# Optimization experiments

Hardware: AMD Instinct MI355X
Metric: run time of the kernel (lower is better)

Reference implementation:

```python
import jax, jax.numpy as jnp
import numpy as np

THRESHOLD = 0.5
N_SEG = 5
NEG_INF = -1e30
EPS = 1e-12  # F.normalize eps


def setup_inputs() -> dict:
    key = jax.random.key(0)
    kx, kl = jax.random.split(key)
    B, D, L = 4096, 512, 80
    x = jax.random.normal(kx, (B, D), dtype=jnp.float32)
    labels = jax.random.randint(kl, (B, L), 0, 2, dtype=jnp.int32)
    return {"x": x, "labels": labels}


def reference(x, labels):
    B = x.shape[0]
    labels_f = labels.astype(jnp.float32)
    # pairwise Jaccard over multi-hot labels
    intersection = labels_f @ labels_f.T                      # [B, B]
    counts = labels_f.sum(axis=1, keepdims=True)              # [B, 1]
    union = counts + counts.T - intersection
    jaccard = intersection / union                            # [B, B]
    # cosine similarity (F.normalize with eps clamp)
    norm = jnp.maximum(jnp.linalg.norm(x, axis=1, keepdims=True), EPS)
    nx = x / norm
    sim = nx @ nx.T                                           # [B, B]
    # --- sample positive (uniform among jaccard > threshold), fixed key ---
    pos_mask = jaccard > THRESHOLD
    valid_mask = jnp.any(pos_mask, axis=1)                    # [B]
    logits = jnp.where(pos_mask, 0.0, NEG_INF)
    sampled = jax.random.categorical(jax.random.key(42), logits, axis=-1)
    pos_samples = jnp.where(valid_mask, sampled, 0)           # invalid rows -> 0
    # --- top-k negatives: jaccard strictly below the positive's jaccard ---
    pos_sim_j = jaccard[jnp.arange(B), pos_samples]           # [B]
    neg_mask = jaccard < pos_sim_j[:, None]
    neg_sims = jnp.where(neg_mask, jaccard, -jnp.inf)
    _, neg_samples = jax.lax.top_k(neg_sims, N_SEG)           # [B, N_SEG]
    # --- contrastive loss on cosine sims at sampled indices ---
    rel_pos = sim[jnp.arange(B), pos_samples]                 # [B]
    rel_neg = jnp.take_along_axis(sim, neg_samples, axis=1)   # [B, N_SEG]
    exp_pos = jnp.exp(rel_pos)
    sum_exp_neg = jnp.exp(rel_neg).sum(axis=1)
    loss = -jnp.log(exp_pos / (exp_pos + sum_exp_neg))
    vm = valid_mask.astype(x.dtype)
    return (loss * vm).sum() / vm.sum()
```

## Files before the change

kernel.cpp:

```cpp
#include <hip/hip_runtime.h>
#include <stdint.h>

#define B_ROWS 4096
#define DIMS   512
#define NLAB   80
#define HALF_ROWS 2048
#define HCNT   8388608u
#define CHUNK  1024
#define SEGCAP 256u

typedef unsigned long long u64;

__device__ __forceinline__ uint32_t rotl32(uint32_t x, uint32_t d) {
    return (x << d) | (x >> (32u - d));
}

__device__ __forceinline__ void tf2x32_key42(uint32_t c0, uint32_t c1,
                                             uint32_t& o0, uint32_t& o1) {
    const uint32_t ks0 = 0u;
    const uint32_t ks1 = 42u;
    const uint32_t ks2 = 0x1BD11BDAu ^ 0u ^ 42u;
    uint32_t x0 = c0 + ks0;
    uint32_t x1 = c1 + ks1;
#define TF_RND(r) { x0 += x1; x1 = rotl32(x1, (r)); x1 ^= x0; }
    TF_RND(13u) TF_RND(15u) TF_RND(26u) TF_RND(6u)
    x0 += ks1; x1 += ks2 + 1u;
    TF_RND(17u) TF_RND(29u) TF_RND(16u) TF_RND(24u)
    x0 += ks2; x1 += ks0 + 2u;
    TF_RND(13u) TF_RND(15u) TF_RND(26u) TF_RND(6u)
    x0 += ks0; x1 += ks1 + 3u;
    TF_RND(17u) TF_RND(29u) TF_RND(16u) TF_RND(24u)
    x0 += ks1; x1 += ks2 + 4u;
    TF_RND(13u) TF_RND(15u) TF_RND(26u) TF_RND(6u)
    x0 += ks2; x1 += ks0 + 5u;
#undef TF_RND
    o0 = x0; o1 = x1;
}

__device__ __forceinline__ u64 shflx64(u64 v, int m) {
    uint32_t lo = __shfl_xor((uint32_t)(v & 0xFFFFFFFFull), m, 64);
    uint32_t hi = __shfl_xor((uint32_t)(v >> 32), m, 64);
    return ((u64)hi << 32) | (u64)lo;
}

__device__ __forceinline__ uint32_t umx(uint32_t a, uint32_t b) { return a > b ? a : b; }
__device__ __forceinline__ uint32_t umn(uint32_t a, uint32_t b) { return a < b ? a : b; }

__device__ __forceinline__ void ins5_u32(uint32_t* t, uint32_t k) {
    t[4] = umx(t[4], k);
    uint32_t hi, lo;
    hi = umx(t[3], t[4]); lo = umn(t[3], t[4]); t[3] = hi; t[4] = lo;
    hi = umx(t[2], t[3]); lo = umn(t[2], t[3]); t[2] = hi; t[3] = lo;
    hi = umx(t[1], t[2]); lo = umn(t[1], t[2]); t[1] = hi; t[2] = lo;
    hi = umx(t[0], t[1]); lo = umn(t[0], t[1]); t[0] = hi; t[1] = lo;
}

__device__ __forceinline__ void merge5_u32(uint32_t* A, const uint32_t* Bv) {
    uint32_t a0=A[0],a1=A[1],a2=A[2],a3=A[3],a4=A[4];
    uint32_t b0=Bv[0],b1=Bv[1],b2=Bv[2],b3=Bv[3],b4=Bv[4];
    uint32_t m0 = umx(a0, b0);
    uint32_t m1 = umx(umx(a1, b1), umn(a0, b0));
    uint32_t m2 = umx(umx(a2, b2), umx(umn(a0, b1), umn(a1, b0)));
    uint32_t m3 = umx(umx(a3, b3), umx(umx(umn(a0, b2), umn(a1, b1)), umn(a2, b0)));
    uint32_t m4 = umx(umx(a4, b4), umx(umx(umn(a0, b3), umn(a1, b2)),
                                       umx(umn(a2, b1), umn(a3, b0))));
    A[0]=m0; A[1]=m1; A[2]=m2; A[3]=m3; A[4]=m4;
}

__device__ __forceinline__ uint32_t jkey19(uint32_t it, uint32_t u) {
    const uint32_t n = it << 19;
    float f = (float)it * __builtin_amdgcn_rcpf((float)u) * 524288.0f;
    uint32_t ak = (uint32_t)f;
    int r = (int)(n - ak * u);
    if (r < 0) { ak--; r += (int)u; }
    if (r >= (int)u) ak++;
    return ak + 1u;
}


__global__ __launch_bounds__(256) void prep_kernel(const float* __restrict__ x,
                                                   const int* __restrict__ labels,
                                                   uint4* __restrict__ pk,
                                                   float* __restrict__ norms) {
    const int tid = threadIdx.x;
    const int lane = tid & 63;
    const int row = blockIdx.x * 4 + (tid >> 6);
    const int* lr = labels + (size_t)row * NLAB;
    const int la = lr[lane];
    const int lb = (lane < 16) ? lr[64 + lane] : 0;
    const u64 b0 = __ballot(la != 0);
    const u64 b1 = __ballot(lb != 0);
    const uint32_t w2 = (uint32_t)b1 & 0xFFFFu;
    const uint32_t cnt = (uint32_t)__popcll(b0) + (uint32_t)__popc(w2);
    if (lane == 0) pk[row] = make_uint4((uint32_t)b0, (uint32_t)(b0 >> 32), w2, cnt);
    const float* xr = x + (size_t)row * DIMS;
    float ss = 0.f;
#pragma unroll
    for (int u = 0; u < 8; ++u) { float v = xr[lane + 64 * u]; ss += v * v; }
#pragma unroll
    for (int m = 1; m < 64; m <<= 1) ss += __shfl_xor(ss, m, 64);
    if (lane == 0) norms[row] = fmaxf(sqrtf(ss), 1e-12f);
}

__global__ __launch_bounds__(256) void fused_kernel(const float* __restrict__ x,
                                                    const uint4* __restrict__ pk,
                                                    const float* __restrict__ norms,
                                                    float2* __restrict__ blockPart) {
    __shared__ uint32_t segL[2][4][SEGCAP];
    __shared__ uint32_t cntL[2][4];
    __shared__ uint32_t keysL[2][4][5];
    __shared__ uint32_t tgL[2][6];
    __shared__ uint32_t validL[2];
    __shared__ float    simsL[2][6];
    __shared__ float    lossW[2], cntW2[2];

    const int tid = threadIdx.x;
    const int lane = tid & 63;
    const int sub  = tid >> 6;
    const int pr   = (int)blockIdx.x;
    const int r0 = pr, r1 = pr + HALF_ROWS;
    const uint4 P0 = pk[r0], P1 = pk[r1];
    const uint32_t cw0 = P0.w, cw1 = P1.w;
    const int jbase = sub * CHUNK;

    uint32_t cnt0 = 0u, cnt1 = 0u;
    uint32_t t0[5], t1[5];
#pragma unroll
    for (int k = 0; k < 5; ++k) {
        const uint32_t fk = (uint32_t)(~(jbase + k)) & 0xFFFu;
        t0[k] = fk; t1[k] = fk;
    }
    uint32_t thr0 = umx(t0[4] >> 12, 1u) - 1u;
    uint32_t thr1 = umx(t1[4] >> 12, 1u) - 1u;

#pragma unroll 4
    for (int jb = 0; jb < CHUNK; jb += 64) {
        const int j = jbase + jb + lane;
        const uint4 pj = pk[j];
        const uint32_t cj = pj.w;
        const uint32_t jx = (~(uint32_t)j) & 0xFFFu;
        const uint32_t it0 = (uint32_t)(__popc(P0.x & pj.x) + __popc(P0.y & pj.y) + __popc(P0.z & pj.z));
        const uint32_t u0  = cw0 + cj - it0;
        const uint32_t it1 = (uint32_t)(__popc(P1.x & pj.x) + __popc(P1.y & pj.y) + __popc(P1.z & pj.z));
        const uint32_t u1  = cw1 + cj - it1;
        const bool c0 = (it0 << 1) > u0;
        const bool c1 = (it1 << 1) > u1;
        const u64 bal0 = __ballot(c0);
        const u64 bal1 = __ballot(c1);
        const u64 lmask = (1ull << lane) - 1ull;
        if (c0) {
            const uint32_t off = cnt0 + (uint32_t)__popcll(bal0 & lmask);
            if (off < SEGCAP) segL[0][sub][off] = (it0 << 20) | (u0 << 12) | (uint32_t)j;
        } else if ((it0 << 19) >= __umul24(thr0, u0)) {
            ins5_u32(t0, (jkey19(it0, u0) << 12) | jx);
            thr0 = umx(t0[4] >> 12, 1u) - 1u;
        }
        cnt0 += (uint32_t)__popcll(bal0);
        if (c1) {
            const uint32_t off = cnt1 + (uint32_t)__popcll(bal1 & lmask);
            if (off < SEGCAP) segL[1][sub][off] = (it1 << 20) | (u1 << 12) | (uint32_t)j;
        } else if ((it1 << 19) >= __umul24(thr1, u1)) {
            ins5_u32(t1, (jkey19(it1, u1) << 12) | jx);
            thr1 = umx(t1[4] >> 12, 1u) - 1u;
        }
        cnt1 += (uint32_t)__popcll(bal1);
    }
#pragma unroll
    for (int m = 1; m < 64; m <<= 1) {
        uint32_t o[5];
#pragma unroll
        for (int k = 0; k < 5; ++k) o[k] = __shfl_xor(t0[k], m, 64);
        merge5_u32(t0, o);
#pragma unroll
        for (int k = 0; k < 5; ++k) o[k] = __shfl_xor(t1[k], m, 64);
        merge5_u32(t1, o);
    }
    if (lane == 0) {
        cntL[0][sub] = cnt0; cntL[1][sub] = cnt1;
#pragma unroll
        for (int k = 0; k < 5; ++k) { keysL[0][sub][k] = t0[k]; keysL[1][sub][k] = t1[k]; }
    }
    __syncthreads();

    if (sub < 2) {
        const int h = sub;
        uint32_t f[5];
#pragma unroll
        for (int k = 0; k < 5; ++k) f[k] = keysL[h][0][k];
#pragma unroll
        for (int s = 1; s < 4; ++s) {
            uint32_t o[5];
#pragma unroll
            for (int k = 0; k < 5; ++k) o[k] = keysL[h][s][k];
            merge5_u32(f, o);
        }
        uint32_t ns[4];
#pragma unroll
        for (int s = 0; s < 4; ++s) ns[s] = umn(cntL[h][s], SEGCAP);

        const uint32_t base23 = (uint32_t)pr * (uint32_t)B_ROWS;
        u64 gb = 0ull;
#pragma unroll
        for (int s = 0; s < 4; ++s) {
            for (int e = lane; e < (int)ns[s]; e += 64) {
                const uint32_t ent = segL[h][s][e];
                const uint32_t j  = ent & 0xFFFu;
                const uint32_t u  = (ent >> 12) & 0xFFu;
                const uint32_t it = ent >> 20;
                uint32_t o0, o1;
                tf2x32_key42(base23 + j, base23 + j + HCNT, o0, o1);
                const uint32_t o = h ? o1 : o0;
                const u64 key = ((u64)(o >> 9) << 41) | ((u64)((~j) & 0xFFFu) << 29) | (u64)jkey19(it, u);
                if (key > gb) gb = key;
            }
        }
#pragma unroll
        for (int m = 1; m < 64; m <<= 1) {
            const u64 o = shflx64(gb, m);
            if (o > gb) gb = o;
        }
        const bool valid = gb != 0ull;
        const int pos = valid ? (int)((~(uint32_t)(gb >> 29)) & 0xFFFu) : 0;
        const uint32_t pjkey = (uint32_t)(gb & 0xFFFFFu);

        uint32_t ts[5] = {0u, 0u, 0u, 0u, 0u};
#pragma unroll
        for (int s = 0; s < 4; ++s) {
            for (int e = lane; e < (int)ns[s]; e += 64) {
                const uint32_t ent = segL[h][s][e];
                const uint32_t j  = ent & 0xFFFu;
                const uint32_t u  = (ent >> 12) & 0xFFu;
                const uint32_t it = ent >> 20;
                const uint32_t k19 = jkey19(it, u);
                if (k19 < pjkey) ins5_u32(ts, (k19 << 12) | ((~j) & 0xFFFu));
            }
        }
#pragma unroll
        for (int m = 1; m < 64; m <<= 1) {
            uint32_t o[5];
#pragma unroll
            for (int k = 0; k < 5; ++k) o[k] = __shfl_xor(ts[k], m, 64);
            merge5_u32(ts, o);
        }
        merge5_u32(f, ts);

        if (lane == 0) {
            tgL[h][0] = (uint32_t)pos;
#pragma unroll
            for (int k = 0; k < 5; ++k) tgL[h][k + 1] = (~f[k]) & 0xFFFu;
            validL[h] = valid ? 1u : 0u;
        }
    }
    __syncthreads();

#pragma unroll
    for (int k = 0; k < 3; ++k) {
        const int d = sub + 4 * k;
        const int h = (d >= 6) ? 1 : 0;
        const int q = d - 6 * h;
        const int row = h ? r1 : r0;
        const int tgt = (int)tgL[h][q];
        const float* pa = x + (size_t)row * DIMS;
        const float* pb = x + (size_t)tgt * DIMS;
        float s = 0.f;
#pragma unroll
        for (int u = 0; u < 8; ++u) s += pa[lane + 64 * u] * pb[lane + 64 * u];
#pragma unroll
        for (int m = 1; m < 64; m <<= 1) s += __shfl_xor(s, m, 64);
        if (lane == 0) simsL[h][q] = s;
    }
    __syncthreads();

    if (sub < 2 && lane == 0) {
        const int h = sub;
        float loss = 0.f, cnt = 0.f;
        if (validL[h]) {
            const int row = h ? r1 : r0;
            const float nr = norms[row];
            const float sp = simsL[h][0] / (nr * norms[tgL[h][0]]);
            float sen = 0.f;
#pragma unroll
            for (int q = 1; q < 6; ++q) sen += expf(simsL[h][q] / (nr * norms[tgL[h][q]]));
            const float ep = expf(sp);
            loss = -logf(ep / (ep + sen));
            cnt = 1.f;
        }
        lossW[h] = loss; cntW2[h] = cnt;
    }
    __syncthreads();
    if (tid == 0) blockPart[pr] = make_float2(lossW[0] + lossW[1], cntW2[0] + cntW2[1]);
}

__global__ __launch_bounds__(256) void final_kernel(const float2* __restrict__ blockPart,
                                                    float* __restrict__ out) {
    __shared__ float rl[4], rc[4];
    const int tid = threadIdx.x;
    const int lane = tid & 63;
    const int w = tid >> 6;
    float sl = 0.f, sc = 0.f;
#pragma unroll
    for (int k = 0; k < 8; ++k) {
        const float2 p = blockPart[tid + 256 * k];
        sl += p.x; sc += p.y;
    }
#pragma unroll
    for (int m = 1; m < 64; m <<= 1) {
        sl += __shfl_xor(sl, m, 64);
        sc += __shfl_xor(sc, m, 64);
    }
    if (lane == 0) { rl[w] = sl; rc[w] = sc; }
    __syncthreads();
    if (tid == 0) out[0] = (rl[0] + rl[1] + rl[2] + rl[3]) / (rc[0] + rc[1] + rc[2] + rc[3]);
}

extern "C" void kernel_launch(void* const* d_in, const int* in_sizes, int n_in,
                              void* d_out, int out_size, void* d_ws, size_t ws_size,
                              hipStream_t stream) {
    const float* x      = (const float*)d_in[0];
    const int*   labels = (const int*)d_in[1];
    float* out = (float*)d_out;

    char* ws = (char*)d_ws;
    uint4*  pk    = (uint4*)ws;
    float*  norms = (float*)(ws + 65536);
    float2* bPart = (float2*)(ws + 65536 + 16384);

    hipLaunchKernelGGL(prep_kernel,  dim3(1024), dim3(256), 0, stream, x, labels, pk, norms);
    hipLaunchKernelGGL(fused_kernel, dim3(2048), dim3(256), 0, stream, x, pk, norms, bPart);
    hipLaunchKernelGGL(final_kernel, dim3(1),    dim3(256), 0, stream, bPart, out);
}
```

Baseline: 100.9 us.

## Process one row per block and spread the positive search across all warps

The fused kernel now handles one row per block instead of two, launching twice as many blocks. The positive-sampling and negative top-k scans over the segment list are now spread across all four warps, where before only two warps did them serially over all segments. The row vector is cached in registers for the six dot products. This shortens the serial tail inside each block and raises parallelism, at the cost of reloading the pk scan data per row and an extra block barrier.

```diff
diff --git a/kernel.cpp b/kernel.cpp
--- a/kernel.cpp
+++ b/kernel.cpp
@@ -105,193 +105,176 @@
 __global__ __launch_bounds__(256) void fused_kernel(const float* __restrict__ x,
                                                     const uint4* __restrict__ pk,
                                                     const float* __restrict__ norms,
-                                                    float2* __restrict__ blockPart) {
-    __shared__ uint32_t segL[2][4][SEGCAP];
-    __shared__ uint32_t cntL[2][4];
-    __shared__ uint32_t keysL[2][4][5];
-    __shared__ uint32_t tgL[2][6];
-    __shared__ uint32_t validL[2];
-    __shared__ float    simsL[2][6];
-    __shared__ float    lossW[2], cntW2[2];
+                                                    float2* __restrict__ rowPart) {
+    __shared__ uint32_t segL[4][SEGCAP];
+    __shared__ uint32_t cntL[4];
+    __shared__ uint32_t keysL[4][5];
+    __shared__ u64      gbL[4];
+    __shared__ uint32_t tsL[4][5];
+    __shared__ float    simsL[6];
 
     const int tid = threadIdx.x;
     const int lane = tid & 63;
     const int sub  = tid >> 6;
-    const int pr   = (int)blockIdx.x;
-    const int r0 = pr, r1 = pr + HALF_ROWS;
-    const uint4 P0 = pk[r0], P1 = pk[r1];
-    const uint32_t cw0 = P0.w, cw1 = P1.w;
+    const int row  = (int)blockIdx.x;
+    const int pr   = row & (HALF_ROWS - 1);
+    const int half = row >> 11;
+    const uint4 P = pk[row];
+    const uint32_t cw = P.w;
     const int jbase = sub * CHUNK;
 
-    uint32_t cnt0 = 0u, cnt1 = 0u;
-    uint32_t t0[5], t1[5];
-#pragma unroll
-    for (int k = 0; k < 5; ++k) {
-        const uint32_t fk = (uint32_t)(~(jbase + k)) & 0xFFFu;
-        t0[k] = fk; t1[k] = fk;
-    }
-    uint32_t thr0 = umx(t0[4] >> 12, 1u) - 1u;
-    uint32_t thr1 = umx(t1[4] >> 12, 1u) - 1u;
+    uint32_t cnt = 0u;
+    uint32_t t[5];
+#pragma unroll
+    for (int k = 0; k < 5; ++k) t[k] = (uint32_t)(~(jbase + k)) & 0xFFFu;
+    uint32_t thr = umx(t[4] >> 12, 1u) - 1u;
 
 #pragma unroll 4
     for (int jb = 0; jb < CHUNK; jb += 64) {
         const int j = jbase + jb + lane;
         const uint4 pj = pk[j];
-        const uint32_t cj = pj.w;
-        const uint32_t jx = (~(uint32_t)j) & 0xFFFu;
-        const uint32_t it0 = (uint32_t)(__popc(P0.x & pj.x) + __popc(P0.y & pj.y) + __popc(P0.z & pj.z));
-        const uint32_t u0  = cw0 + cj - it0;
-        const uint32_t it1 = (uint32_t)(__popc(P1.x & pj.x) + __popc(P1.y & pj.y) + __popc(P1.z & pj.z));
-        const uint32_t u1  = cw1 + cj - it1;
-        const bool c0 = (it0 << 1) > u0;
-        const bool c1 = (it1 << 1) > u1;
-        const u64 bal0 = __ballot(c0);
-        const u64 bal1 = __ballot(c1);
-        const u64 lmask = (1ull << lane) - 1ull;
-        if (c0) {
-            const uint32_t off = cnt0 + (uint32_t)__popcll(bal0 & lmask);
-            if (off < SEGCAP) segL[0][sub][off] = (it0 << 20) | (u0 << 12) | (uint32_t)j;
-        } else if ((it0 << 19) >= __umul24(thr0, u0)) {
-            ins5_u32(t0, (jkey19(it0, u0) << 12) | jx);
-            thr0 = umx(t0[4] >> 12, 1u) - 1u;
+        const uint32_t it = (uint32_t)(__popc(P.x & pj.x) + __popc(P.y & pj.y) + __popc(P.z & pj.z));
+        const uint32_t u  = cw + pj.w - it;
+        const bool c = (it << 1) > u;
+        const u64 bal = __ballot(c);
+        if (c) {
+            const uint32_t off = cnt + (uint32_t)__popcll(bal & ((1ull << lane) - 1ull));
+            if (off < SEGCAP) segL[sub][off] = (it << 20) | (u << 12) | (uint32_t)j;
+        } else if ((it << 19) >= __umul24(thr, u)) {
+            ins5_u32(t, (jkey19(it, u) << 12) | ((~(uint32_t)j) & 0xFFFu));
+            thr = umx(t[4] >> 12, 1u) - 1u;
         }
-        cnt0 += (uint32_t)__popcll(bal0);
-        if (c1) {
-            const uint32_t off = cnt1 + (uint32_t)__popcll(bal1 & lmask);
-            if (off < SEGCAP) segL[1][sub][off] = (it1 << 20) | (u1 << 12) | (uint32_t)j;
-        } else if ((it1 << 19) >= __umul24(thr1, u1)) {
-            ins5_u32(t1, (jkey19(it1, u1) << 12) | jx);
-            thr1 = umx(t1[4] >> 12, 1u) - 1u;
-        }
-        cnt1 += (uint32_t)__popcll(bal1);
+        cnt += (uint32_t)__popcll(bal);
     }
 #pragma unroll
     for (int m = 1; m < 64; m <<= 1) {
         uint32_t o[5];
 #pragma unroll
-        for (int k = 0; k < 5; ++k) o[k] = __shfl_xor(t0[k], m, 64);
-        merge5_u32(t0, o);
-#pragma unroll
-        for (int k = 0; k < 5; ++k) o[k] = __shfl_xor(t1[k], m, 64);
-        merge5_u32(t1, o);
+        for (int k = 0; k < 5; ++k) o[k] = __shfl_xor(t[k], m, 64);
+        merge5_u32(t, o);
     }
     if (lane == 0) {
-        cntL[0][sub] = cnt0; cntL[1][sub] = cnt1;
-#pragma unroll
-        for (int k = 0; k < 5; ++k) { keysL[0][sub][k] = t0[k]; keysL[1][sub][k] = t1[k]; }
-    }
-    __syncthreads();
-
+        cntL[sub] = cnt;
+#pragma unroll
+        for (int k = 0; k < 5; ++k) keysL[sub][k] = t[k];
+    }
+    __syncthreads();
+
+    const uint32_t nseg = umn(cntL[sub], SEGCAP);
+    const uint32_t base23 = (uint32_t)pr * (uint32_t)B_ROWS;
+    u64 gb = 0ull;
+    for (int e = lane; e < (int)nseg; e += 64) {
+        const uint32_t ent = segL[sub][e];
+        const uint32_t j  = ent & 0xFFFu;
+        const uint32_t u  = (ent >> 12) & 0xFFu;
+        const uint32_t it = ent >> 20;
+        uint32_t o0, o1;
+        tf2x32_key42(base23 + j, base23 + j + HCNT, o0, o1);
+        const uint32_t o = half ? o1 : o0;
+        const u64 key = ((u64)(o >> 9) << 41) | ((u64)((~j) & 0xFFFu) << 29) | (u64)jkey19(it, u);
+        if (key > gb) gb = key;
+    }
+#pragma unroll
+    for (int m = 1; m < 64; m <<= 1) {
+        const u64 o = shflx64(gb, m);
+        if (o > gb) gb = o;
+    }
+    if (lane == 0) gbL[sub] = gb;
+    __syncthreads();
+    u64 GB = gbL[0];
+#pragma unroll
+    for (int s = 1; s < 4; ++s) { const u64 o = gbL[s]; if (o > GB) GB = o; }
+    const bool valid = GB != 0ull;
+    const int pos = valid ? (int)((~(uint32_t)(GB >> 29)) & 0xFFFu) : 0;
+    const uint32_t pjkey = (uint32_t)(GB & 0xFFFFFu);
+
+    uint32_t ts[5] = {0u, 0u, 0u, 0u, 0u};
+    for (int e = lane; e < (int)nseg; e += 64) {
+        const uint32_t ent = segL[sub][e];
+        const uint32_t j  = ent & 0xFFFu;
+        const uint32_t u  = (ent >> 12) & 0xFFu;
+        const uint32_t it = ent >> 20;
+        const uint32_t k19 = jkey19(it, u);
+        if (k19 < pjkey) ins5_u32(ts, (k19 << 12) | ((~j) & 0xFFFu));
+    }
+#pragma unroll
+    for (int m = 1; m < 64; m <<= 1) {
+        uint32_t o[5];
+#pragma unroll
+        for (int k = 0; k < 5; ++k) o[k] = __shfl_xor(ts[k], m, 64);
+        merge5_u32(ts, o);
+    }
+    if (lane == 0) {
+#pragma unroll
+        for (int k = 0; k < 5; ++k) tsL[sub][k] = ts[k];
+    }
+    __syncthreads();
+
+    uint32_t f[5];
+#pragma unroll
+    for (int k = 0; k < 5; ++k) f[k] = keysL[0][k];
+#pragma unroll
+    for (int s = 1; s < 4; ++s) {
+        uint32_t o[5];
+#pragma unroll
+        for (int k = 0; k < 5; ++k) o[k] = keysL[s][k];
+        merge5_u32(f, o);
+    }
+#pragma unroll
+    for (int s = 0; s < 4; ++s) {
+        uint32_t o[5];
+#pragma unroll
+        for (int k = 0; k < 5; ++k) o[k] = tsL[s][k];
+        merge5_u32(f, o);
+    }
+    int tg[6];
+    tg[0] = pos;
+#pragma unroll
+    for (int k = 0; k < 5; ++k) tg[k + 1] = (int)((~f[k]) & 0xFFFu);
+
+    const float* xr = x + (size_t)row * DIMS;
+    float v[8];
+#pragma unroll
+    for (int u = 0; u < 8; ++u) v[u] = xr[lane + 64 * u];
+    {
+        const int q = sub;
+        const float* pb = x + (size_t)tg[q] * DIMS;
+        float s = 0.f;
+#pragma unroll
+        for (int u = 0; u < 8; ++u) s += v[u] * pb[lane + 64 * u];
+#pragma unroll
+        for (int m = 1; m < 64; m <<= 1) s += __shfl_xor(s, m, 64);
+        if (lane == 0) simsL[q] = s;
+    }
     if (sub < 2) {
-        const int h = sub;
-        uint32_t f[5];
-#pragma unroll
-        for (int k = 0; k < 5; ++k) f[k] = keysL[h][0][k];
-#pragma unroll
-        for (int s = 1; s < 4; ++s) {
-            uint32_t o[5];
-#pragma unroll
-            for (int k = 0; k < 5; ++k) o[k] = keysL[h][s][k];
-            merge5_u32(f, o);
-        }
-        uint32_t ns[4];
-#pragma unroll
-        for (int s = 0; s < 4; ++s) ns[s] = umn(cntL[h][s], SEGCAP);
-
-        const uint32_t base23 = (uint32_t)pr * (uint32_t)B_ROWS;
-        u64 gb = 0ull;
-#pragma unroll
-        for (int s = 0; s < 4; ++s) {
-            for (int e = lane; e < (int)ns[s]; e += 64) {
-                const uint32_t ent = segL[h][s][e];
-                const uint32_t j  = ent & 0xFFFu;
-                const uint32_t u  = (ent >> 12) & 0xFFu;
-                const uint32_t it = ent >> 20;
-                uint32_t o0, o1;
-                tf2x32_key42(base23 + j, base23 + j + HCNT, o0, o1);
-                const uint32_t o = h ? o1 : o0;
-                const u64 key = ((u64)(o >> 9) << 41) | ((u64)((~j) & 0xFFFu) << 29) | (u64)jkey19(it, u);
-                if (key > gb) gb = key;
-            }
-        }
-#pragma unroll
-        for (int m = 1; m < 64; m <<= 1) {
-            const u64 o = shflx64(gb, m);
-            if (o > gb) gb = o;
-        }
-        const bool valid = gb != 0ull;
-        const int pos = valid ? (int)((~(uint32_t)(gb >> 29)) & 0xFFFu) : 0;
-        const uint32_t pjkey = (uint32_t)(gb & 0xFFFFFu);
-
-        uint32_t ts[5] = {0u, 0u, 0u, 0u, 0u};
-#pragma unroll
-        for (int s = 0; s < 4; ++s) {
-            for (int e = lane; e < (int)ns[s]; e += 64) {
-                const uint32_t ent = segL[h][s][e];
-                const uint32_t j  = ent & 0xFFFu;
-                const uint32_t u  = (ent >> 12) & 0xFFu;
-                const uint32_t it = ent >> 20;
-                const uint32_t k19 = jkey19(it, u);
-                if (k19 < pjkey) ins5_u32(ts, (k19 << 12) | ((~j) & 0xFFFu));
-            }
-        }
-#pragma unroll
-        for (int m = 1; m < 64; m <<= 1) {
-            uint32_t o[5];
-#pragma unroll
-            for (int k = 0; k < 5; ++k) o[k] = __shfl_xor(ts[k], m, 64);
-            merge5_u32(ts, o);
-        }
-        merge5_u32(f, ts);
-
-        if (lane == 0) {
-            tgL[h][0] = (uint32_t)pos;
-#pragma unroll
-            for (int k = 0; k < 5; ++k) tgL[h][k + 1] = (~f[k]) & 0xFFFu;
-            validL[h] = valid ? 1u : 0u;
-        }
-    }
-    __syncthreads();
-
-#pragma unroll
-    for (int k = 0; k < 3; ++k) {
-        const int d = sub + 4 * k;
-        const int h = (d >= 6) ? 1 : 0;
-        const int q = d - 6 * h;
-        const int row = h ? r1 : r0;
-        const int tgt = (int)tgL[h][q];
-        const float* pa = x + (size_t)row * DIMS;
-        const float* pb = x + (size_t)tgt * DIMS;
+        const int q = 4 + sub;
+        const float* pb = x + (size_t)tg[q] * DIMS;
         float s = 0.f;
 #pragma unroll
-        for (int u = 0; u < 8; ++u) s += pa[lane + 64 * u] * pb[lane + 64 * u];
+        for (int u = 0; u < 8; ++u) s += v[u] * pb[lane + 64 * u];
 #pragma unroll
         for (int m = 1; m < 64; m <<= 1) s += __shfl_xor(s, m, 64);
-        if (lane == 0) simsL[h][q] = s;
-    }
-    __syncthreads();
-
-    if (sub < 2 && lane == 0) {
-        const int h = sub;
-        float loss = 0.f, cnt = 0.f;
-        if (validL[h]) {
-            const int row = h ? r1 : r0;
+        if (lane == 0) simsL[q] = s;
+    }
+    __syncthreads();
+
+    if (tid == 0) {
+        float loss = 0.f, c = 0.f;
+        if (valid) {
             const float nr = norms[row];
-            const float sp = simsL[h][0] / (nr * norms[tgL[h][0]]);
+            const float sp = simsL[0] / (nr * norms[tg[0]]);
             float sen = 0.f;
 #pragma unroll
-            for (int q = 1; q < 6; ++q) sen += expf(simsL[h][q] / (nr * norms[tgL[h][q]]));
+            for (int q = 1; q < 6; ++q) sen += expf(simsL[q] / (nr * norms[tg[q]]));
             const float ep = expf(sp);
             loss = -logf(ep / (ep + sen));
-            cnt = 1.f;
+            c = 1.f;
         }
-        lossW[h] = loss; cntW2[h] = cnt;
-    }
-    __syncthreads();
-    if (tid == 0) blockPart[pr] = make_float2(lossW[0] + lossW[1], cntW2[0] + cntW2[1]);
-}
-
-__global__ __launch_bounds__(256) void final_kernel(const float2* __restrict__ blockPart,
+        rowPart[row] = make_float2(loss, c);
+    }
+}
+
+__global__ __launch_bounds__(256) void final_kernel(const float2* __restrict__ rowPart,
                                                     float* __restrict__ out) {
     __shared__ float rl[4], rc[4];
     const int tid = threadIdx.x;
@@ -299,8 +282,8 @@
     const int w = tid >> 6;
     float sl = 0.f, sc = 0.f;
 #pragma unroll
-    for (int k = 0; k < 8; ++k) {
-        const float2 p = blockPart[tid + 256 * k];
+    for (int k = 0; k < 16; ++k) {
+        const float2 p = rowPart[tid + 256 * k];
         sl += p.x; sc += p.y;
     }
 #pragma unroll
@@ -323,9 +306,9 @@
     char* ws = (char*)d_ws;
     uint4*  pk    = (uint4*)ws;
     float*  norms = (float*)(ws + 65536);
-    float2* bPart = (float2*)(ws + 65536 + 16384);
+    float2* rPart = (float2*)(ws + 65536 + 16384);
 
     hipLaunchKernelGGL(prep_kernel,  dim3(1024), dim3(256), 0, stream, x, labels, pk, norms);
-    hipLaunchKernelGGL(fused_kernel, dim3(2048), dim3(256), 0, stream, x, pk, norms, bPart);
-    hipLaunchKernelGGL(final_kernel, dim3(1),    dim3(256), 0, stream, bPart, out);
-}
+    hipLaunchKernelGGL(fused_kernel, dim3(4096), dim3(256), 0, stream, x, pk, norms, rPart);
+    hipLaunchKernelGGL(final_kernel, dim3(1),    dim3(256), 0, stream, rPart, out);
+}
```

Result: slower. 104.9 us (+4.0%).

## Spread positive sampling and negative top-k across all four wavefronts

Applied to the files above, without the earlier changes.

The per-row positive sampling (Threefry hashing over candidate segments) and the filtered top-5 negative selection previously ran in only two wavefronts, each looping over all four segments. Now every wavefront handles its own segment for both rows, with partial maxima and top-5 lists exchanged through shared memory and merged afterward. This removes the serialized tail where half the block sat idle. It also raises the occupancy hint in launch bounds and unrolls the scan loop further, at the cost of two extra barriers and possible register pressure.

```diff
diff --git a/kernel.cpp b/kernel.cpp
--- a/kernel.cpp
+++ b/kernel.cpp
@@ -102,13 +102,15 @@
     if (lane == 0) norms[row] = fmaxf(sqrtf(ss), 1e-12f);
 }
 
-__global__ __launch_bounds__(256) void fused_kernel(const float* __restrict__ x,
-                                                    const uint4* __restrict__ pk,
-                                                    const float* __restrict__ norms,
-                                                    float2* __restrict__ blockPart) {
+__global__ __launch_bounds__(256, 8) void fused_kernel(const float* __restrict__ x,
+                                                       const uint4* __restrict__ pk,
+                                                       const float* __restrict__ norms,
+                                                       float2* __restrict__ blockPart) {
     __shared__ uint32_t segL[2][4][SEGCAP];
     __shared__ uint32_t cntL[2][4];
     __shared__ uint32_t keysL[2][4][5];
+    __shared__ u64      gbL[2][4];
+    __shared__ uint32_t tsL[2][4][5];
     __shared__ uint32_t tgL[2][6];
     __shared__ uint32_t validL[2];
     __shared__ float    simsL[2][6];
@@ -133,7 +135,7 @@
     uint32_t thr0 = umx(t0[4] >> 12, 1u) - 1u;
     uint32_t thr1 = umx(t1[4] >> 12, 1u) - 1u;
 
-#pragma unroll 4
+#pragma unroll 8
     for (int jb = 0; jb < CHUNK; jb += 64) {
         const int j = jbase + jb + lane;
         const uint4 pj = pk[j];
@@ -182,6 +184,82 @@
     }
     __syncthreads();
 
+    const uint32_t ns0 = umn(cntL[0][sub], SEGCAP);
+    const uint32_t ns1 = umn(cntL[1][sub], SEGCAP);
+    const uint32_t base23 = (uint32_t)pr * (uint32_t)B_ROWS;
+    u64 gb0 = 0ull, gb1 = 0ull;
+    for (int e = lane; e < (int)ns0; e += 64) {
+        const uint32_t ent = segL[0][sub][e];
+        const uint32_t j  = ent & 0xFFFu;
+        const uint32_t u  = (ent >> 12) & 0xFFu;
+        const uint32_t it = ent >> 20;
+        uint32_t o0, o1;
+        tf2x32_key42(base23 + j, base23 + j + HCNT, o0, o1);
+        const u64 key = ((u64)(o0 >> 9) << 41) | ((u64)((~j) & 0xFFFu) << 29) | (u64)jkey19(it, u);
+        if (key > gb0) gb0 = key;
+    }
+    for (int e = lane; e < (int)ns1; e += 64) {
+        const uint32_t ent = segL[1][sub][e];
+        const uint32_t j  = ent & 0xFFFu;
+        const uint32_t u  = (ent >> 12) & 0xFFu;
+        const uint32_t it = ent >> 20;
+        uint32_t o0, o1;
+        tf2x32_key42(base23 + j, base23 + j + HCNT, o0, o1);
+        const u64 key = ((u64)(o1 >> 9) << 41) | ((u64)((~j) & 0xFFFu) << 29) | (u64)jkey19(it, u);
+        if (key > gb1) gb1 = key;
+    }
+#pragma unroll
+    for (int m = 1; m < 64; m <<= 1) {
+        const u64 o0 = shflx64(gb0, m), o1 = shflx64(gb1, m);
+        if (o0 > gb0) gb0 = o0;
+        if (o1 > gb1) gb1 = o1;
+    }
+    if (lane == 0) { gbL[0][sub] = gb0; gbL[1][sub] = gb1; }
+    __syncthreads();
+    u64 GB0 = gbL[0][0], GB1 = gbL[1][0];
+#pragma unroll
+    for (int s = 1; s < 4; ++s) {
+        const u64 o0 = gbL[0][s], o1 = gbL[1][s];
+        if (o0 > GB0) GB0 = o0;
+        if (o1 > GB1) GB1 = o1;
+    }
+    const bool valid0 = GB0 != 0ull, valid1 = GB1 != 0ull;
+    const uint32_t pjkey0 = (uint32_t)(GB0 & 0xFFFFFu);
+    const uint32_t pjkey1 = (uint32_t)(GB1 & 0xFFFFFu);
+
+    uint32_t ts0[5] = {0u,0u,0u,0u,0u}, ts1[5] = {0u,0u,0u,0u,0u};
+    for (int e = lane; e < (int)ns0; e += 64) {
+        const uint32_t ent = segL[0][sub][e];
+        const uint32_t j  = ent & 0xFFFu;
+        const uint32_t u  = (ent >> 12) & 0xFFu;
+        const uint32_t it = ent >> 20;
+        const uint32_t k19 = jkey19(it, u);
+        if (k19 < pjkey0) ins5_u32(ts0, (k19 << 12) | ((~j) & 0xFFFu));
+    }
+    for (int e = lane; e < (int)ns1; e += 64) {
+        const uint32_t ent = segL[1][sub][e];
+        const uint32_t j  = ent & 0xFFFu;
+        const uint32_t u  = (ent >> 12) & 0xFFu;
+        const uint32_t it = ent >> 20;
+        const uint32_t k19 = jkey19(it, u);
+        if (k19 < pjkey1) ins5_u32(ts1, (k19 << 12) | ((~j) & 0xFFFu));
+    }
+#pragma unroll
+    for (int m = 1; m < 64; m <<= 1) {
+        uint32_t o[5];
+#pragma unroll
+        for (int k = 0; k < 5; ++k) o[k] = __shfl_xor(ts0[k], m, 64);
+        merge5_u32(ts0, o);
+#pragma unroll
+        for (int k = 0; k < 5; ++k) o[k] = __shfl_xor(ts1[k], m, 64);
+        merge5_u32(ts1, o);
+    }
+    if (lane == 0) {
+#pragma unroll
+        for (int k = 0; k < 5; ++k) { tsL[0][sub][k] = ts0[k]; tsL[1][sub][k] = ts1[k]; }
+    }
+    __syncthreads();
+
     if (sub < 2) {
         const int h = sub;
         uint32_t f[5];
@@ -194,58 +272,17 @@
             for (int k = 0; k < 5; ++k) o[k] = keysL[h][s][k];
             merge5_u32(f, o);
         }
-        uint32_t ns[4];
-#pragma unroll
-        for (int s = 0; s < 4; ++s) ns[s] = umn(cntL[h][s], SEGCAP);
-
-        const uint32_t base23 = (uint32_t)pr * (uint32_t)B_ROWS;
-        u64 gb = 0ull;
 #pragma unroll
         for (int s = 0; s < 4; ++s) {
-            for (int e = lane; e < (int)ns[s]; e += 64) {
-                const uint32_t ent = segL[h][s][e];
-                const uint32_t j  = ent & 0xFFFu;
-                const uint32_t u  = (ent >> 12) & 0xFFu;
-                const uint32_t it = ent >> 20;
-                uint32_t o0, o1;
-                tf2x32_key42(base23 + j, base23 + j + HCNT, o0, o1);
-                const uint32_t o = h ? o1 : o0;
-                const u64 key = ((u64)(o >> 9) << 41) | ((u64)((~j) & 0xFFFu) << 29) | (u64)jkey19(it, u);
-                if (key > gb) gb = key;
-            }
-        }
-#pragma unroll
-        for (int m = 1; m < 64; m <<= 1) {
-            const u64 o = shflx64(gb, m);
-            if (o > gb) gb = o;
-        }
-        const bool valid = gb != 0ull;
-        const int pos = valid ? (int)((~(uint32_t)(gb >> 29)) & 0xFFFu) : 0;
-        const uint32_t pjkey = (uint32_t)(gb & 0xFFFFFu);
-
-        uint32_t ts[5] = {0u, 0u, 0u, 0u, 0u};
-#pragma unroll
-        for (int s = 0; s < 4; ++s) {
-            for (int e = lane; e < (int)ns[s]; e += 64) {
-                const uint32_t ent = segL[h][s][e];
-                const uint32_t j  = ent & 0xFFFu;
-                const uint32_t u  = (ent >> 12) & 0xFFu;
-                const uint32_t it = ent >> 20;
-                const uint32_t k19 = jkey19(it, u);
-                if (k19 < pjkey) ins5_u32(ts, (k19 << 12) | ((~j) & 0xFFFu));
-            }
-        }
-#pragma unroll
-        for (int m = 1; m < 64; m <<= 1) {
             uint32_t o[5];
 #pragma unroll
-            for (int k = 0; k < 5; ++k) o[k] = __shfl_xor(ts[k], m, 64);
-            merge5_u32(ts, o);
-        }
-        merge5_u32(f, ts);
-
+            for (int k = 0; k < 5; ++k) o[k] = tsL[h][s][k];
+            merge5_u32(f, o);
+        }
         if (lane == 0) {
-            tgL[h][0] = (uint32_t)pos;
+            const u64 GB = h ? GB1 : GB0;
+            const bool valid = h ? valid1 : valid0;
+            tgL[h][0] = valid ? ((~(uint32_t)(GB >> 29)) & 0xFFFu) : 0u;
 #pragma unroll
             for (int k = 0; k < 5; ++k) tgL[h][k + 1] = (~f[k]) & 0xFFFu;
             validL[h] = valid ? 1u : 0u;
```

Measured after the change: 103.5 us. 2.6% more time.
